# Optimization experiments

Hardware: AMD Instinct MI355X
Metric: run time of the kernel (lower is better)

## Reference

```python
import jax, jax.numpy as jnp
import numpy as np

B, S, D, H = 4, 1024, 1024, 16
E = 8                 # num_experts
FF1 = 4096            # d_hidden * expansion_factor * 2 (swiglu in)
FF2 = 2048            # d_hidden * expansion_factor (swiglu out / linear2 in)
TEMP = 0.5            # gating temperature
RMS_EPS_GATE = float(np.finfo(np.float32).eps)  # torch RMSNorm default eps
NORM_EPS = 1e-8       # layer_norm_eps


def setup_inputs() -> dict:
    key = jax.random.key(0)
    ks = jax.random.split(key, 8)
    s = 0.02
    return {
        "x": jax.random.normal(ks[0], (B, S, D), jnp.float32),
        "w_qkv": jax.random.normal(ks[1], (3 * D, D), jnp.float32) * s,
        "w_out": jax.random.normal(ks[2], (D, D), jnp.float32) * s,
        "norm1_w": jnp.ones((D,), jnp.float32),
        "norm2_w": jnp.ones((D,), jnp.float32),
        "gate_w": jax.random.normal(ks[3], (E, D), jnp.float32) * s,
        "gate_b": jnp.zeros((E,), jnp.float32),
        "gate_rms_w": jnp.ones((E,), jnp.float32),
        "w1": jax.random.normal(ks[4], (E, D, FF1), jnp.float32) * s,
        "w2": jax.random.normal(ks[5], (E, FF2, D), jnp.float32) * s,
    }


def _rmsnorm(x, w, eps):
    return x * w * jax.lax.rsqrt(jnp.mean(x * x, axis=-1, keepdims=True) + eps)


def _attn(h, w_qkv, w_out):
    qkv = h @ w_qkv.T                              # [B,S,3D]
    q, k, v = jnp.split(qkv, 3, axis=-1)
    dh = D // H
    q = q.reshape(B, S, H, dh)
    k = k.reshape(B, S, H, dh)
    v = v.reshape(B, S, H, dh)
    scores = jnp.einsum("bqhd,bkhd->bhqk", q, k) / jnp.sqrt(jnp.float32(dh))
    p = jax.nn.softmax(scores, axis=-1)
    o = jnp.einsum("bhqk,bkhd->bqhd", p, v).reshape(B, S, D)
    return o @ w_out.T


def _moe(h, gate_w, gate_b, gate_rms_w, w1, w2):
    xf = h.reshape(-1, D)                          # [N,D]
    logits = _rmsnorm(xf @ gate_w.T + gate_b, gate_rms_w, RMS_EPS_GATE)
    gates = jax.nn.softmax(logits / TEMP, axis=-1)  # [N,E]
    top_g, _ = jax.lax.top_k(gates, 1)              # top_k = 1
    # capacity dispatch mask degenerates to all-ones (capacity >= 1), so
    # normalized gate = g / (g + 1e-6)
    g = top_g[:, 0] / (top_g[:, 0] + 1e-6)          # [N]
    h1 = jnp.einsum("nd,edf->nef", xf, w1)          # [N,E,FF1]
    a, b = jnp.split(h1, 2, axis=-1)                # SwiGLU
    act = a * jax.nn.silu(b)                        # [N,E,FF2]
    outs = jnp.einsum("nef,efd->ned", act, w2)      # [N,E,D]
    # gate broadcasts over the expert axis (as in the original code)
    comb = outs.sum(axis=1) * g[:, None]
    return comb.reshape(h.shape)


def reference(x, w_qkv, w_out, norm1_w, norm2_w, gate_w, gate_b, gate_rms_w, w1, w2):
    # pre-norm transformer block, eval mode (no dropout / gating noise)
    x = x + _attn(_rmsnorm(x, norm1_w, NORM_EPS), w_qkv, w_out)
    x = x + _moe(_rmsnorm(x, norm2_w, NORM_EPS), gate_w, gate_b, gate_rms_w, w1, w2)
    return x
```

## Files before the change

kernel.cpp:

```cpp
#include <hip/hip_runtime.h>
#include <hip/hip_bf16.h>
#include <math.h>

typedef __bf16 bf16_t;
typedef __bf16 bf16x8 __attribute__((ext_vector_type(8)));
typedef float f32x4 __attribute__((ext_vector_type(4)));

typedef const __attribute__((address_space(1))) void* gptr_t;
typedef __attribute__((address_space(3))) void* lptr_t;

#define MFMA16(a, b, c) __builtin_amdgcn_mfma_f32_16x16x32_bf16((a), (b), (c), 0, 0, 0)
#define BAR() __builtin_amdgcn_s_barrier()
#define WAIT_LGKM()                                        \
  do {                                                     \
    asm volatile("s_waitcnt lgkmcnt(0)" ::: "memory");     \
    __builtin_amdgcn_sched_barrier(0);                     \
  } while (0)
#define WAIT_VM4()                                         \
  do {                                                     \
    asm volatile("s_waitcnt vmcnt(4)" ::: "memory");       \
    __builtin_amdgcn_sched_barrier(0);                     \
  } while (0)

__device__ __forceinline__ void gload_lds16(const bf16_t* g, bf16_t* l) {
  __builtin_amdgcn_global_load_lds((gptr_t)g, (lptr_t)l, 16, 0, 0);
}

__global__ __launch_bounds__(256) void conv_kernel(const float* __restrict__ in,
                                                   bf16_t* __restrict__ out, int n4) {
  int i = blockIdx.x * 256 + threadIdx.x;
  if (i >= n4) return;
  float4 v = ((const float4*)in)[i];
  bf16_t* o = out + (size_t)i * 4;
  o[0] = (bf16_t)v.x; o[1] = (bf16_t)v.y; o[2] = (bf16_t)v.z; o[3] = (bf16_t)v.w;
}

__global__ __launch_bounds__(256) void transp_w1(const float* __restrict__ in,
                                                 bf16_t* __restrict__ out) {
  __shared__ float tile[32][33];
  const float* ip = in + (size_t)blockIdx.z * 1024 * 4096;
  bf16_t* op = out + (size_t)blockIdx.z * 4096 * 1024;
  int tx = threadIdx.x, ty = threadIdx.y;
  int r0 = blockIdx.y * 32, c0 = blockIdx.x * 32;
#pragma unroll
  for (int i = 0; i < 32; i += 8)
    tile[ty + i][tx] = ip[(size_t)(r0 + ty + i) * 4096 + c0 + tx];
  __syncthreads();
#pragma unroll
  for (int i = 0; i < 32; i += 8) {
    int c = c0 + ty + i;
    int p = (c < 2048) ? ((c >> 5) * 64 + (c & 31))
                       : (((c - 2048) >> 5) * 64 + 32 + ((c - 2048) & 31));
    op[(size_t)p * 1024 + r0 + tx] = (bf16_t)tile[tx][ty + i];
  }
}

__global__ __launch_bounds__(256) void transp_w2(const float* __restrict__ in,
                                                 bf16_t* __restrict__ out) {
  __shared__ float tile[32][33];
  const float* ip = in + (size_t)blockIdx.z * 2048 * 1024;
  int tx = threadIdx.x, ty = threadIdx.y;
  int r0 = blockIdx.y * 32, c0 = blockIdx.x * 32;
#pragma unroll
  for (int i = 0; i < 32; i += 8)
    tile[ty + i][tx] = ip[(size_t)(r0 + ty + i) * 1024 + c0 + tx];
  __syncthreads();
#pragma unroll
  for (int i = 0; i < 32; i += 8)
    out[(size_t)(c0 + ty + i) * 16384 + blockIdx.z * 2048 + r0 + tx] = (bf16_t)tile[tx][ty + i];
}

__global__ __launch_bounds__(256) void rmsnorm_kernel(const float* __restrict__ x,
                                                      const float* __restrict__ w,
                                                      bf16_t* __restrict__ out, float eps) {
  int row = blockIdx.x;
  int t = threadIdx.x;
  const float4* xr = (const float4*)(x + (size_t)row * 1024);
  float4 v = xr[t];
  float ss = v.x * v.x + v.y * v.y + v.z * v.z + v.w * v.w;
#pragma unroll
  for (int off = 1; off < 64; off <<= 1) ss += __shfl_xor(ss, off, 64);
  __shared__ float red[4];
  int wave = t >> 6, lane = t & 63;
  if (lane == 0) red[wave] = ss;
  __syncthreads();
  ss = red[0] + red[1] + red[2] + red[3];
  float inv = rsqrtf(ss * (1.0f / 1024.0f) + eps);
  float4 wv = ((const float4*)w)[t];
  bf16_t* o = out + (size_t)row * 1024 + t * 4;
  o[0] = (bf16_t)(v.x * wv.x * inv);
  o[1] = (bf16_t)(v.y * wv.y * inv);
  o[2] = (bf16_t)(v.z * wv.z * inv);
  o[3] = (bf16_t)(v.w * wv.w * inv);
}

template <int EPI>
__global__ __launch_bounds__(512, 2) void gemm256(const bf16_t* __restrict__ A,
                                                  const bf16_t* __restrict__ Bt,
                                                  void* __restrict__ C,
                                                  const float* __restrict__ resid,
                                                  int M, int N, int K, int lda, int ldb) {
  __shared__ bf16_t As[2][256 * 64];
  __shared__ bf16_t Bs[2][256 * 64];
  const int tid = threadIdx.x;
  const int wave = tid >> 6, lane = tid & 63;
  const int m0 = blockIdx.y * 256, n0 = blockIdx.x * 256;
  const int wr = (wave >> 2) * 128, wc = (wave & 3) * 64;
  const int fr = lane & 15, fq = lane >> 4;

  if (EPI == 4) Bt += (size_t)blockIdx.z * 4096 * 1024;
  if (EPI == 5) {
    A += (size_t)blockIdx.z * K;
    Bt += (size_t)blockIdx.z * K;
  }

  const int srw = lane >> 3;
  const int sgc = (lane & 7) ^ srw;
  const bf16_t* aBase = A + (size_t)(m0 + wave * 8 + srw) * lda + sgc * 8;
  const bf16_t* bBase = Bt + (size_t)(n0 + wave * 8 + srw) * ldb + sgc * 8;

  auto stageA = [&](bf16_t* buf, int kt, int h) {
#pragma unroll
    for (int i = 0; i < 2; ++i) {
      int r = h * 128 + i * 64;
      gload_lds16(aBase + (size_t)r * lda + kt * 64, &buf[(r + wave * 8) * 64]);
    }
  };
  auto stageB = [&](bf16_t* buf, int kt, int h) {
#pragma unroll
    for (int i = 0; i < 2; ++i) {
      int r = h * 128 + i * 64;
      gload_lds16(bBase + (size_t)r * ldb + kt * 64, &buf[(r + wave * 8) * 64]);
    }
  };

  f32x4 acc[8][4] = {};
  bf16x8 a_[4][2], b_[4][2];

  auto readA = [&](int b, int mh) {
#pragma unroll
    for (int q = 0; q < 4; ++q)
#pragma unroll
      for (int ks = 0; ks < 2; ++ks) {
        int r = wr + mh * 64 + q * 16 + fr;
        a_[q][ks] = *(const bf16x8*)&As[b][r * 64 + (((fq + ks * 4) ^ (fr & 7)) << 3)];
      }
  };
  auto readB = [&](int b, int nh) {
#pragma unroll
    for (int q = 0; q < 2; ++q)
#pragma unroll
      for (int ks = 0; ks < 2; ++ks) {
        int r = wc + nh * 32 + q * 16 + fr;
        b_[nh * 2 + q][ks] = *(const bf16x8*)&Bs[b][r * 64 + (((fq + ks * 4) ^ (fr & 7)) << 3)];
      }
  };
  auto mfma16x = [&](int mh, int nh) {
    __builtin_amdgcn_s_setprio(1);
#pragma unroll
    for (int q = 0; q < 4; ++q)
#pragma unroll
      for (int n = 0; n < 2; ++n)
#pragma unroll
        for (int ks = 0; ks < 2; ++ks)
          acc[mh * 4 + q][nh * 2 + n] =
              MFMA16(a_[q][ks], b_[nh * 2 + n][ks], acc[mh * 4 + q][nh * 2 + n]);
    __builtin_amdgcn_s_setprio(0);
  };

  const int NKT = K >> 6;
  stageB(Bs[0], 0, 0);
  stageA(As[0], 0, 0);
  stageA(As[0], 0, 1);
  stageB(Bs[0], 0, 1);
  stageB(Bs[1], 1, 0);
  stageA(As[1], 1, 0);
  WAIT_VM4();
  BAR();

  for (int it = 0; it < (NKT >> 1); ++it) {
    const int t1s = 2 * it + 1;
    int t2 = 2 * it + 2; if (t2 >= NKT) t2 -= NKT;
    int t3 = 2 * it + 3; if (t3 >= NKT) t3 -= NKT;
    readA(0, 0); readB(0, 0);
    stageA(As[1], t1s, 1);
    BAR(); WAIT_LGKM(); mfma16x(0, 0); BAR();
    readB(0, 1);
    stageB(Bs[1], t1s, 1);
    BAR(); WAIT_LGKM(); mfma16x(0, 1); BAR();
    readA(0, 1);
    stageB(Bs[0], t2, 0);
    BAR(); WAIT_LGKM(); mfma16x(1, 0); BAR();
    stageA(As[0], t2, 0);
    BAR(); mfma16x(1, 1);
    WAIT_VM4();
    BAR();
    readA(1, 0); readB(1, 0);
    stageA(As[0], t2, 1);
    BAR(); WAIT_LGKM(); mfma16x(0, 0); BAR();
    readB(1, 1);
    stageB(Bs[0], t2, 1);
    BAR(); WAIT_LGKM(); mfma16x(0, 1); BAR();
    readA(1, 1);
    stageB(Bs[1], t3, 0);
    BAR(); WAIT_LGKM(); mfma16x(1, 0); BAR();
    stageA(As[1], t3, 0);
    BAR(); mfma16x(1, 1);
    WAIT_VM4();
    BAR();
  }

  if (EPI == 4) {
    bf16_t* act = (bf16_t*)C;
    int strip = (n0 >> 6) + (wave & 3);
#pragma unroll
    for (int mq = 0; mq < 8; ++mq)
#pragma unroll
      for (int n = 0; n < 2; ++n)
#pragma unroll
        for (int j = 0; j < 4; ++j) {
          size_t row = (size_t)(m0 + wr + mq * 16 + fq * 4 + j);
          size_t col = (size_t)blockIdx.z * 2048 + strip * 32 + n * 16 + fr;
          float a = acc[mq][n][j], b = acc[mq][n + 2][j];
          act[row * 16384 + col] = (bf16_t)(a * (b / (1.0f + __expf(-b))));
        }
    return;
  }
#pragma unroll
  for (int mq = 0; mq < 8; ++mq)
#pragma unroll
    for (int n = 0; n < 4; ++n)
#pragma unroll
      for (int j = 0; j < 4; ++j) {
        size_t row = (size_t)(m0 + wr + mq * 16 + fq * 4 + j);
        size_t col = (size_t)(n0 + wc + n * 16 + fr);
        float v = acc[mq][n][j];
        if (EPI == 0)
          ((bf16_t*)C)[row * N + col] = (bf16_t)v;
        else if (EPI == 1)
          ((float*)C)[row * N + col] = resid[row * N + col] + v;
        else if (EPI == 5)
          ((float*)C + (size_t)blockIdx.z * M * N)[row * N + col] = v;
      }
}

__global__ __launch_bounds__(256) void attn_kernel(const bf16_t* __restrict__ qkv,
                                                   bf16_t* __restrict__ o) {
  const int S = 1024, LD = 3072;
  int qt = blockIdx.x, bh = blockIdx.y;
  int b = bh >> 4, h = bh & 15;
  int tid = threadIdx.x, wave = tid >> 6, lane = tid & 63;
  int fr = lane & 15, fq = lane >> 4, kg = fq * 8;
  int q0 = qt * 64 + wave * 16;
  const bf16_t* qb = qkv + (size_t)b * S * LD + h * 64;
  const bf16_t* kb = qb + 1024;
  const bf16_t* vb = qb + 2048;

  __shared__ bf16_t Ks[64 * 64];
  __shared__ bf16_t Vt[64 * 64];
  __shared__ bf16_t Ps[4][16 * 72];

  bf16x8 qf0 = *(const bf16x8*)&qb[(size_t)(q0 + fr) * LD + kg];
  bf16x8 qf1 = *(const bf16x8*)&qb[(size_t)(q0 + fr) * LD + 32 + kg];

  f32x4 acc[4] = {};
  float mrow[4] = {-1e30f, -1e30f, -1e30f, -1e30f};
  float ssum[4] = {0.f, 0.f, 0.f, 0.f};

  for (int k0 = 0; k0 < S; k0 += 64) {
#pragma unroll
    for (int cc = 0; cc < 2; ++cc) {
      int c = tid + cc * 256;
      int r = c >> 3, ch = c & 7;
      *(bf16x8*)&Ks[r * 64 + ((ch ^ (r & 7)) << 3)] =
          *(const bf16x8*)&kb[(size_t)(k0 + r) * LD + ch * 8];
      bf16x8 vv = *(const bf16x8*)&vb[(size_t)(k0 + r) * LD + ch * 8];
#pragma unroll
      for (int i = 0; i < 8; ++i) {
        int d = ch * 8 + i;
        int cs = ((r >> 3) ^ (d >> 3) ^ (d & 7)) & 7;
        Vt[d * 64 + cs * 8 + (r & 7)] = vv[i];
      }
    }
    __syncthreads();

    f32x4 s[4];
#pragma unroll
    for (int kc = 0; kc < 4; ++kc) {
      int row = kc * 16 + fr, sw = row & 7;
      bf16x8 kf0 = *(const bf16x8*)&Ks[row * 64 + ((fq ^ sw) << 3)];
      bf16x8 kf1 = *(const bf16x8*)&Ks[row * 64 + (((4 + fq) ^ sw) << 3)];
      f32x4 z = {};
      z = MFMA16(qf0, kf0, z);
      z = MFMA16(qf1, kf1, z);
      s[kc] = z * 0.125f;
    }
    float pmax[4], psum[4], scl[4];
#pragma unroll
    for (int j = 0; j < 4; ++j)
      pmax[j] = fmaxf(fmaxf(s[0][j], s[1][j]), fmaxf(s[2][j], s[3][j]));
#pragma unroll
    for (int off = 1; off < 16; off <<= 1)
#pragma unroll
      for (int j = 0; j < 4; ++j) pmax[j] = fmaxf(pmax[j], __shfl_xor(pmax[j], off, 64));
#pragma unroll
    for (int j = 0; j < 4; ++j) {
      float nm = fmaxf(mrow[j], pmax[j]);
      scl[j] = __expf(mrow[j] - nm);
      mrow[j] = nm;
      psum[j] = 0.f;
    }
#pragma unroll
    for (int kc = 0; kc < 4; ++kc)
#pragma unroll
      for (int j = 0; j < 4; ++j) {
        float p = __expf(s[kc][j] - mrow[j]);
        psum[j] += p;
        Ps[wave][(fq * 4 + j) * 72 + kc * 16 + fr] = (bf16_t)p;
      }
#pragma unroll
    for (int off = 1; off < 16; off <<= 1)
#pragma unroll
      for (int j = 0; j < 4; ++j) psum[j] += __shfl_xor(psum[j], off, 64);
#pragma unroll
    for (int j = 0; j < 4; ++j) ssum[j] = ssum[j] * scl[j] + psum[j];
#pragma unroll
    for (int n = 0; n < 4; ++n)
#pragma unroll
      for (int j = 0; j < 4; ++j) acc[n][j] *= scl[j];
    asm volatile("s_waitcnt lgkmcnt(0)" ::: "memory");
    bf16x8 pa[2];
#pragma unroll
    for (int ks = 0; ks < 2; ++ks) pa[ks] = *(const bf16x8*)&Ps[wave][fr * 72 + ks * 32 + kg];
#pragma unroll
    for (int n = 0; n < 4; ++n) {
      int d = n * 16 + fr;
      int swd = ((d >> 3) ^ (d & 7)) & 7;
#pragma unroll
      for (int ks = 0; ks < 2; ++ks) {
        bf16x8 vbf = *(const bf16x8*)&Vt[d * 64 + (((ks * 4 + fq) ^ swd) << 3)];
        acc[n] = MFMA16(pa[ks], vbf, acc[n]);
      }
    }
    __syncthreads();
  }
#pragma unroll
  for (int n = 0; n < 4; ++n)
#pragma unroll
    for (int j = 0; j < 4; ++j) {
      size_t row = (size_t)b * S + q0 + fq * 4 + j;
      o[row * 1024 + h * 64 + n * 16 + fr] = (bf16_t)(acc[n][j] / ssum[j]);
    }
}

__global__ __launch_bounds__(256) void gate_kernel(const bf16_t* __restrict__ hn,
                                                   const float* __restrict__ gw,
                                                   const float* __restrict__ gb,
                                                   const float* __restrict__ grms,
                                                   float* __restrict__ g) {
  int n = blockIdx.x * 4 + (threadIdx.x >> 6);
  int lane = threadIdx.x & 63;
  const bf16_t* xr = hn + (size_t)n * 1024;
  float acc[8] = {};
  for (int i = lane; i < 1024; i += 64) {
    float xv = (float)xr[i];
#pragma unroll
    for (int e = 0; e < 8; ++e) acc[e] += xv * gw[e * 1024 + i];
  }
#pragma unroll
  for (int e = 0; e < 8; ++e)
    for (int off = 1; off < 64; off <<= 1) acc[e] += __shfl_xor(acc[e], off, 64);
  float l[8], ms = 0.f;
#pragma unroll
  for (int e = 0; e < 8; ++e) {
    l[e] = acc[e] + gb[e];
    ms += l[e] * l[e];
  }
  float inv = rsqrtf(ms * 0.125f + 1.1920928955078125e-07f);
  float mx = -1e30f;
#pragma unroll
  for (int e = 0; e < 8; ++e) {
    l[e] = l[e] * inv * grms[e] * 2.0f;
    mx = fmaxf(mx, l[e]);
  }
  float s = 0.f;
#pragma unroll
  for (int e = 0; e < 8; ++e) s += __expf(l[e] - mx);
  float t = 1.0f / s;
  if (lane == 0) g[n] = t / (t + 1e-6f);
}

__global__ __launch_bounds__(256) void combine8(const float* __restrict__ moep,
                                                const float* __restrict__ x1,
                                                const float* __restrict__ g,
                                                float* __restrict__ out, int Mc) {
  size_t i4 = (size_t)blockIdx.x * 256 + threadIdx.x;
  size_t row = i4 >> 8;
  size_t stride4 = (size_t)Mc * 256;
  float4 s = {0.f, 0.f, 0.f, 0.f};
#pragma unroll
  for (int z = 0; z < 8; ++z) {
    float4 v = ((const float4*)moep)[z * stride4 + i4];
    s.x += v.x; s.y += v.y; s.z += v.z; s.w += v.w;
  }
  float gv = g[row];
  float4 xv = ((const float4*)x1)[i4];
  float4 r;
  r.x = xv.x + s.x * gv;
  r.y = xv.y + s.y * gv;
  r.z = xv.z + s.z * gv;
  r.w = xv.w + s.w * gv;
  ((float4*)out)[i4] = r;
}

extern "C" void kernel_launch(void* const* d_in, const int* in_sizes, int n_in,
                              void* d_out, int out_size, void* d_ws, size_t ws_size,
                              hipStream_t stream) {
  const float* x = (const float*)d_in[0];
  const float* w_qkv = (const float*)d_in[1];
  const float* w_out = (const float*)d_in[2];
  const float* norm1_w = (const float*)d_in[3];
  const float* norm2_w = (const float*)d_in[4];
  const float* gate_w = (const float*)d_in[5];
  const float* gate_b = (const float*)d_in[6];
  const float* gate_rms = (const float*)d_in[7];
  const float* w1 = (const float*)d_in[8];
  const float* w2 = (const float*)d_in[9];
  float* out = (float*)d_out;

  const size_t baseB = (8ull * 4096 * 1024 + 1024ull * 16384 + 3072ull * 1024 +
                        1024ull * 1024 + 4096ull * 1024) * 2 +
                       4096ull * 1024 * 4 + 4096 * 4;
  int cc = 4;
  {
    size_t need2 = baseB + 2048ull * 16384 * 2 + 8ull * 2048 * 1024 * 4;
    if (ws_size >= need2) cc = 2;
  }
  const int Mc = 4096 / cc;

  char* ws = (char*)d_ws;
  size_t off = 0;
  auto alloc = [&](size_t bytes) {
    char* p = ws + off;
    off += bytes;
    return p;
  };
  bf16_t* w1t = (bf16_t*)alloc(8ull * 4096 * 1024 * 2);
  bf16_t* w2t = (bf16_t*)alloc(1024ull * 16384 * 2);
  bf16_t* wqkvb = (bf16_t*)alloc(3072ull * 1024 * 2);
  bf16_t* woutb = (bf16_t*)alloc(1024ull * 1024 * 2);
  bf16_t* hn = (bf16_t*)alloc(4096ull * 1024 * 2);
  float* x1 = (float*)alloc(4096ull * 1024 * 4);
  float* gbuf = (float*)alloc(4096ull * 4);
  bf16_t* act = (bf16_t*)alloc((size_t)Mc * 16384 * 2);
  float* moep = (float*)alloc(8ull * Mc * 1024 * 4);
  bf16_t* qkvb = (bf16_t*)act;
  bf16_t* attno = (bf16_t*)moep;

  conv_kernel<<<3072, 256, 0, stream>>>(w_qkv, wqkvb, 3072 * 1024 / 4);
  conv_kernel<<<1024, 256, 0, stream>>>(w_out, woutb, 1024 * 1024 / 4);
  transp_w1<<<dim3(128, 32, 8), dim3(32, 8), 0, stream>>>(w1, w1t);
  transp_w2<<<dim3(32, 64, 8), dim3(32, 8), 0, stream>>>(w2, w2t);

  rmsnorm_kernel<<<4096, 256, 0, stream>>>(x, norm1_w, hn, 1e-8f);
  gemm256<0><<<dim3(12, 16), 512, 0, stream>>>(hn, wqkvb, qkvb, nullptr, 4096, 3072, 1024,
                                               1024, 1024);
  attn_kernel<<<dim3(16, 64), 256, 0, stream>>>(qkvb, attno);
  gemm256<1><<<dim3(4, 16), 512, 0, stream>>>(attno, woutb, x1, x, 4096, 1024, 1024, 1024,
                                              1024);

  rmsnorm_kernel<<<4096, 256, 0, stream>>>(x1, norm2_w, hn, 1e-8f);
  gate_kernel<<<1024, 256, 0, stream>>>(hn, gate_w, gate_b, gate_rms, gbuf);
  for (int c = 0; c < cc; ++c) {
    gemm256<4><<<dim3(16, Mc / 256, 8), 512, 0, stream>>>(
        hn + (size_t)c * Mc * 1024, w1t, act, nullptr, Mc, 4096, 1024, 1024, 1024);
    gemm256<5><<<dim3(4, Mc / 256, 8), 512, 0, stream>>>(
        act, w2t, moep, nullptr, Mc, 1024, 2048, 16384, 16384);
    combine8<<<Mc, 256, 0, stream>>>(moep, x1 + (size_t)c * Mc * 1024, gbuf + (size_t)c * Mc,
                                     out + (size_t)c * Mc * 1024, Mc);
  }
}
```

Baseline: 684.2 us.

## Restructure GEMM prefetch to whole-tile stages, add XCD-aware block remap, allow single chunk

The GEMM main loop now stages full 256x64 A/B tiles one k-step ahead with a vmcnt(8) wait, instead of interleaving half-tile loads. A peeled epilogue iteration replaces the wrap-around loads that previously fetched redundant tiles. Workgroup IDs are remapped so consecutive tiles are grouped per XCD (stride-8 interleave), aiming at better L2 reuse. The MoE chunk count can drop to 1 when the workspace is large enough, cutting launches at the cost of more workspace.

```diff
diff --git a/kernel.cpp b/kernel.cpp
--- a/kernel.cpp
+++ b/kernel.cpp
@@ -16,9 +16,14 @@
     asm volatile("s_waitcnt lgkmcnt(0)" ::: "memory");     \
     __builtin_amdgcn_sched_barrier(0);                     \
   } while (0)
-#define WAIT_VM4()                                         \
+#define WAIT_VM8()                                         \
   do {                                                     \
-    asm volatile("s_waitcnt vmcnt(4)" ::: "memory");       \
+    asm volatile("s_waitcnt vmcnt(8)" ::: "memory");       \
+    __builtin_amdgcn_sched_barrier(0);                     \
+  } while (0)
+#define WAIT_VM0()                                         \
+  do {                                                     \
+    asm volatile("s_waitcnt vmcnt(0)" ::: "memory");       \
     __builtin_amdgcn_sched_barrier(0);                     \
   } while (0)
 
@@ -104,14 +109,23 @@
   __shared__ bf16_t Bs[2][256 * 64];
   const int tid = threadIdx.x;
   const int wave = tid >> 6, lane = tid & 63;
-  const int m0 = blockIdx.y * 256, n0 = blockIdx.x * 256;
+
+  const int gx = gridDim.x, gy = gridDim.y;
+  int nwg = gx * gy * gridDim.z;
+  int lin = blockIdx.x + gx * (blockIdx.y + gy * blockIdx.z);
+  int wid = ((nwg & 7) == 0) ? ((lin & 7) * (nwg >> 3) + (lin >> 3)) : lin;
+  const int bx = wid % gx;
+  const int by = (wid / gx) % gy;
+  const int bz = wid / (gx * gy);
+
+  const int m0 = by * 256, n0 = bx * 256;
   const int wr = (wave >> 2) * 128, wc = (wave & 3) * 64;
   const int fr = lane & 15, fq = lane >> 4;
 
-  if (EPI == 4) Bt += (size_t)blockIdx.z * 4096 * 1024;
+  if (EPI == 4) Bt += (size_t)bz * 4096 * 1024;
   if (EPI == 5) {
-    A += (size_t)blockIdx.z * K;
-    Bt += (size_t)blockIdx.z * K;
+    A += (size_t)bz * K;
+    Bt += (size_t)bz * K;
   }
 
   const int srw = lane >> 3;
@@ -119,17 +133,17 @@
   const bf16_t* aBase = A + (size_t)(m0 + wave * 8 + srw) * lda + sgc * 8;
   const bf16_t* bBase = Bt + (size_t)(n0 + wave * 8 + srw) * ldb + sgc * 8;
 
-  auto stageA = [&](bf16_t* buf, int kt, int h) {
-#pragma unroll
-    for (int i = 0; i < 2; ++i) {
-      int r = h * 128 + i * 64;
+  auto stageA = [&](bf16_t* buf, int kt) {
+#pragma unroll
+    for (int i = 0; i < 4; ++i) {
+      int r = i * 64;
       gload_lds16(aBase + (size_t)r * lda + kt * 64, &buf[(r + wave * 8) * 64]);
     }
   };
-  auto stageB = [&](bf16_t* buf, int kt, int h) {
-#pragma unroll
-    for (int i = 0; i < 2; ++i) {
-      int r = h * 128 + i * 64;
+  auto stageB = [&](bf16_t* buf, int kt) {
+#pragma unroll
+    for (int i = 0; i < 4; ++i) {
+      int r = i * 64;
       gload_lds16(bBase + (size_t)r * ldb + kt * 64, &buf[(r + wave * 8) * 64]);
     }
   };
@@ -169,45 +183,56 @@
   };
 
   const int NKT = K >> 6;
-  stageB(Bs[0], 0, 0);
-  stageA(As[0], 0, 0);
-  stageA(As[0], 0, 1);
-  stageB(Bs[0], 0, 1);
-  stageB(Bs[1], 1, 0);
-  stageA(As[1], 1, 0);
-  WAIT_VM4();
+  stageB(Bs[0], 0);
+  stageA(As[0], 0);
+  stageB(Bs[1], 1);
+  stageA(As[1], 1);
+  WAIT_VM8();
   BAR();
 
-  for (int it = 0; it < (NKT >> 1); ++it) {
-    const int t1s = 2 * it + 1;
-    int t2 = 2 * it + 2; if (t2 >= NKT) t2 -= NKT;
-    int t3 = 2 * it + 3; if (t3 >= NKT) t3 -= NKT;
+  for (int it = 0; it < (NKT >> 1) - 1; ++it) {
+    const int t2 = 2 * it + 2, t3 = 2 * it + 3;
     readA(0, 0); readB(0, 0);
-    stageA(As[1], t1s, 1);
     BAR(); WAIT_LGKM(); mfma16x(0, 0); BAR();
     readB(0, 1);
-    stageB(Bs[1], t1s, 1);
     BAR(); WAIT_LGKM(); mfma16x(0, 1); BAR();
     readA(0, 1);
-    stageB(Bs[0], t2, 0);
+    stageB(Bs[0], t2);
     BAR(); WAIT_LGKM(); mfma16x(1, 0); BAR();
-    stageA(As[0], t2, 0);
+    stageA(As[0], t2);
     BAR(); mfma16x(1, 1);
-    WAIT_VM4();
+    WAIT_VM8();
     BAR();
     readA(1, 0); readB(1, 0);
-    stageA(As[0], t2, 1);
     BAR(); WAIT_LGKM(); mfma16x(0, 0); BAR();
     readB(1, 1);
-    stageB(Bs[0], t2, 1);
     BAR(); WAIT_LGKM(); mfma16x(0, 1); BAR();
     readA(1, 1);
-    stageB(Bs[1], t3, 0);
+    stageB(Bs[1], t3);
     BAR(); WAIT_LGKM(); mfma16x(1, 0); BAR();
-    stageA(As[1], t3, 0);
+    stageA(As[1], t3);
     BAR(); mfma16x(1, 1);
-    WAIT_VM4();
+    WAIT_VM8();
     BAR();
+  }
+
+  {
+    readA(0, 0); readB(0, 0);
+    BAR(); WAIT_LGKM(); mfma16x(0, 0); BAR();
+    readB(0, 1);
+    BAR(); WAIT_LGKM(); mfma16x(0, 1); BAR();
+    readA(0, 1);
+    BAR(); WAIT_LGKM(); mfma16x(1, 0); BAR();
+    BAR(); mfma16x(1, 1);
+    WAIT_VM0();
+    BAR();
+    readA(1, 0); readB(1, 0);
+    BAR(); WAIT_LGKM(); mfma16x(0, 0); BAR();
+    readB(1, 1);
+    BAR(); WAIT_LGKM(); mfma16x(0, 1); BAR();
+    readA(1, 1);
+    BAR(); WAIT_LGKM(); mfma16x(1, 0); BAR();
+    mfma16x(1, 1);
   }
 
   if (EPI == 4) {
@@ -220,7 +245,7 @@
 #pragma unroll
         for (int j = 0; j < 4; ++j) {
           size_t row = (size_t)(m0 + wr + mq * 16 + fq * 4 + j);
-          size_t col = (size_t)blockIdx.z * 2048 + strip * 32 + n * 16 + fr;
+          size_t col = (size_t)bz * 2048 + strip * 32 + n * 16 + fr;
           float a = acc[mq][n][j], b = acc[mq][n + 2][j];
           act[row * 16384 + col] = (bf16_t)(a * (b / (1.0f + __expf(-b))));
         }
@@ -240,7 +265,7 @@
         else if (EPI == 1)
           ((float*)C)[row * N + col] = resid[row * N + col] + v;
         else if (EPI == 5)
-          ((float*)C + (size_t)blockIdx.z * M * N)[row * N + col] = v;
+          ((float*)C + (size_t)bz * M * N)[row * N + col] = v;
       }
 }
 
@@ -432,10 +457,10 @@
                         1024ull * 1024 + 4096ull * 1024) * 2 +
                        4096ull * 1024 * 4 + 4096 * 4;
   int cc = 4;
-  {
-    size_t need2 = baseB + 2048ull * 16384 * 2 + 8ull * 2048 * 1024 * 4;
-    if (ws_size >= need2) cc = 2;
-  }
+  if (ws_size >= baseB + 4096ull * 16384 * 2 + 8ull * 4096 * 1024 * 4)
+    cc = 1;
+  else if (ws_size >= baseB + 2048ull * 16384 * 2 + 8ull * 2048 * 1024 * 4)
+    cc = 2;
   const int Mc = 4096 / cc;
 
   char* ws = (char*)d_ws;
```

Result: faster. 651.6 us (-4.8%).
